# Performance work log

Measured on AMD Instinct MI355X. Metric: run time of the kernel, lower is better.

## Reference

```python
import jax, jax.numpy as jnp
import numpy as np

N, F, H, C, HX, E = 50000, 256, 128, 16, 64, 500000
TEMP = 1.0


def gcn_conv(x, src, dst, W, b, n):
    # PyG GCNConv: x @ W, add self-loops, sym-normalized scatter-sum src->dst
    xw = x @ W
    idx = jnp.arange(n)
    s = jnp.concatenate([src, idx])
    d = jnp.concatenate([dst, idx])
    deg = jax.ops.segment_sum(jnp.ones_like(s, dtype=xw.dtype), d, num_segments=n)
    dinv = jnp.where(deg > 0, jax.lax.rsqrt(deg), 0.0)
    norm = dinv[s] * dinv[d]
    out = jax.ops.segment_sum(xw[s] * norm[:, None], d, num_segments=n)
    return out + b


def setup_inputs() -> dict:
    key = jax.random.key(0)
    ks = jax.random.split(key, 16)
    x = jax.random.normal(ks[0], (N, F), jnp.float32)
    edge_index = jax.random.randint(ks[1], (2, E), 0, N)
    neg_edge_index = jax.random.randint(ks[2], (2, E), 0, N)
    y = jax.random.randint(ks[3], (N,), 0, C)
    train_mask = jax.random.uniform(ks[4], (N,)) < 0.5
    def lin(k, fi, fo):
        s = 1.0 / np.sqrt(fi)
        return jax.random.uniform(k, (fi, fo), jnp.float32, -s, s)
    W1 = lin(ks[5], F, H); b1 = jnp.zeros((H,), jnp.float32)
    W2 = lin(ks[6], H, C); b2 = jnp.zeros((C,), jnp.float32)
    Wx = lin(ks[7], F, HX); bx = jnp.zeros((HX,), jnp.float32)
    Wd = lin(ks[8], 2 * (HX + C), 1); bd = jnp.zeros((1,), jnp.float32)
    return dict(x=x, edge_index=edge_index, neg_edge_index=neg_edge_index, y=y,
                train_mask=train_mask, W1=W1, b1=b1, W2=W2, b2=b2,
                Wx=Wx, bx=bx, Wd=Wd, bd=bd)


def reference(x, edge_index, neg_edge_index, y, train_mask,
              W1, b1, W2, b2, Wx, bx, Wd, bd):
    n = x.shape[0]
    # GNN encoder p(y|x,G): 2-layer GCN (eval mode -> dropout identity)
    h = jax.nn.relu(gcn_conv(x, edge_index[0], edge_index[1], W1, b1, n))
    logits = gcn_conv(h, edge_index[0], edge_index[1], W2, b2, n) / TEMP
    y_log_prob = jax.nn.log_softmax(logits, axis=-1)
    y_prob = jnp.where(train_mask[:, None],
                       jax.nn.one_hot(y, logits.shape[-1], dtype=logits.dtype),
                       jnp.exp(y_log_prob))
    # node feature encoder
    xe = jax.nn.relu(x @ Wx + bx)
    def decode(ei):
        s, d = ei[0], ei[1]
        feat = jnp.concatenate([xe[s], xe[d], y_prob[s], y_prob[d]], axis=1)
        return feat @ Wd + bd
    e_pred_pos = decode(edge_index)
    e_pred_neg = decode(neg_edge_index)
    return e_pred_pos, e_pred_neg, y_log_prob
```

## Files before the change

### kernel.cpp

```cpp
#include <hip/hip_runtime.h>

typedef unsigned short ushort_t;
typedef __attribute__((ext_vector_type(8))) short short8;
typedef __attribute__((ext_vector_type(4))) float floatx4;

constexpr int F = 256, H = 128, C = 16, HX = 64;
constexpr int NBCOL = H + HX;

__device__ __forceinline__ ushort_t f2bf(float f) {
  unsigned u = __float_as_uint(f);
  u += 0x7fffu + ((u >> 16) & 1u);
  return (ushort_t)(u >> 16);
}
__device__ __forceinline__ float bflo(unsigned u) { return __uint_as_float(u << 16); }
__device__ __forceinline__ float bfhi(unsigned u) { return __uint_as_float(u & 0xffff0000u); }

__global__ void k_pre(const float* __restrict__ x, ushort_t* __restrict__ xb, int totalU,
                      const float* __restrict__ W1, const float* __restrict__ Wx,
                      ushort_t* __restrict__ WBt,
                      const int* __restrict__ dst, int* __restrict__ deg, int e,
                      int n, int nbx, int nbw) {
  int b = blockIdx.x;
  if (b < nbx) {
    int i = b * 256 + threadIdx.x;
    if (i >= totalU) return;
    int tile = i >> 9, rem = i & 511, j = rem >> 4, l15 = rem & 15;
    int row = tile * 16 + l15;
    ushort4 lo = make_ushort4(0, 0, 0, 0), hi = lo;
    if (row < n) {
      const float4* xp = (const float4*)(x + (size_t)row * F + j * 8);
      float4 a = xp[0], bb = xp[1];
      lo = make_ushort4(f2bf(a.x), f2bf(a.y), f2bf(a.z), f2bf(a.w));
      hi = make_ushort4(f2bf(bb.x), f2bf(bb.y), f2bf(bb.z), f2bf(bb.w));
    }
    ((ushort4*)xb)[2 * i] = lo;
    ((ushort4*)xb)[2 * i + 1] = hi;
  } else if (b < nbx + nbw) {
    int i = (b - nbx) * 256 + threadIdx.x;
    if (i >= NBCOL * F) return;
    int nn = i / F, k = i % F;
    float v = (nn < H) ? W1[k * H + nn] : Wx[k * HX + (nn - H)];
    WBt[nn * F + k] = f2bf(v);
  } else {
    int i = (b - nbx - nbw) * 256 + threadIdx.x;
    if (i < e) atomicAdd(&deg[dst[i]], 1);
  }
}

__global__ void k_scan_a(const int* __restrict__ deg, int* __restrict__ part, int n) {
  __shared__ int sm[256];
  int i = blockIdx.x * 256 + threadIdx.x;
  int v = (i < n) ? deg[i] : 0;
  sm[threadIdx.x] = v;
  __syncthreads();
  for (int s = 128; s > 0; s >>= 1) {
    if (threadIdx.x < s) sm[threadIdx.x] += sm[threadIdx.x + s];
    __syncthreads();
  }
  if (threadIdx.x == 0) part[blockIdx.x] = sm[0];
}

__global__ void k_scan_c(const int* __restrict__ deg, const int* __restrict__ part,
                         int* __restrict__ row_start, int* __restrict__ cursor,
                         float* __restrict__ dinv, int n, int e) {
  __shared__ int psm[256];
  __shared__ int wsum[4], woff[4];
  int c = blockIdx.x, t = threadIdx.x;
  psm[t] = (t < c) ? part[t] : 0;
  __syncthreads();
  for (int s = 128; s > 0; s >>= 1) {
    if (t < s) psm[t] += psm[t + s];
    __syncthreads();
  }
  int blockoff = psm[0];
  __syncthreads();

  int i = c * 256 + t;
  int lane = t & 63, wid = t >> 6;
  int v = (i < n) ? deg[i] : 0;
  int xs = v;
  for (int d = 1; d < 64; d <<= 1) {
    int u = __shfl_up(xs, d);
    if (lane >= d) xs += u;
  }
  if (lane == 63) wsum[wid] = xs;
  __syncthreads();
  if (t == 0) {
    int s = 0;
    for (int w = 0; w < 4; w++) { woff[w] = s; s += wsum[w]; }
  }
  __syncthreads();
  int excl = xs - v + woff[wid] + blockoff;
  if (i < n) {
    row_start[i] = excl;
    cursor[i] = excl;
    dinv[i] = rsqrtf((float)(v + 1));
  }
  if (i == 0) row_start[n] = e;
}

__global__ void k_fill(const int* __restrict__ src, const int* __restrict__ dst,
                       const float* __restrict__ dinv, int* __restrict__ cursor,
                       int2* __restrict__ csr8, int e) {
  int i = blockIdx.x * 256 + threadIdx.x;
  if (i < e) {
    int s = src[i];
    int p = atomicAdd(&cursor[dst[i]], 1);
    csr8[p] = make_int2(s, __float_as_int(dinv[s]));
  }
}

__global__ __launch_bounds__(256, 3) void k_gemm1(const ushort_t* __restrict__ xb,
                                                  const ushort_t* __restrict__ WBt,
                                                  const float* __restrict__ bx,
                                                  ushort_t* __restrict__ xw1,
                                                  float* __restrict__ xe,
                                                  int n, int ntiles) {
  int w = threadIdx.x >> 6, lane = threadIdx.x & 63;
  int q = lane >> 4, l15 = lane & 15;
  const short8* bb = (const short8*)WBt;
  short8 bfr[3][8];
#pragma unroll
  for (int t = 0; t < 3; t++)
#pragma unroll
    for (int kk = 0; kk < 8; kk++)
      bfr[t][kk] = bb[(size_t)(w * 48 + t * 16 + l15) * 32 + kk * 4 + q];

  float bxv[3];
#pragma unroll
  for (int t = 0; t < 3; t++) {
    int g = w * 48 + t * 16;
    bxv[t] = (g >= H) ? bx[g - H + l15] : 0.0f;
  }

  const short8* ab = (const short8*)xb;
  for (int tile = blockIdx.x; tile < ntiles; tile += gridDim.x) {
    const short8* atile = ab + (size_t)tile * 512;
    short8 a[8];
#pragma unroll
    for (int kk = 0; kk < 8; kk++) a[kk] = atile[kk * 64 + q * 16 + l15];

    floatx4 acc0 = (floatx4)(0.0f), acc1 = (floatx4)(0.0f), acc2 = (floatx4)(0.0f);
#pragma unroll
    for (int kk = 0; kk < 8; kk++) {
      acc0 = __builtin_amdgcn_mfma_f32_16x16x32_bf16(a[kk], bfr[0][kk], acc0, 0, 0, 0);
      acc1 = __builtin_amdgcn_mfma_f32_16x16x32_bf16(a[kk], bfr[1][kk], acc1, 0, 0, 0);
      acc2 = __builtin_amdgcn_mfma_f32_16x16x32_bf16(a[kk], bfr[2][kk], acc2, 0, 0, 0);
    }

    floatx4 accs[3] = {acc0, acc1, acc2};
    int rbase = tile * 16 + q * 4;
#pragma unroll
    for (int t = 0; t < 3; t++) {
      int g = w * 48 + t * 16;
#pragma unroll
      for (int r = 0; r < 4; r++) {
        int ro = rbase + r;
        if (ro < n) {
          if (g < H) {
            xw1[(size_t)ro * H + g + l15] = f2bf(accs[t][r]);
          } else {
            xe[(size_t)ro * HX + (g - H) + l15] = fmaxf(accs[t][r] + bxv[t], 0.0f);
          }
        }
      }
    }
  }
}

__global__ void k_agg1g2(const ushort_t* __restrict__ xw1, const int* __restrict__ row_start,
                         const int2* __restrict__ csr8, const float* __restrict__ dinv,
                         const float* __restrict__ b1, const float* __restrict__ W2,
                         float* __restrict__ hw2, int n) {
  __shared__ float2 hsm[4][64];
  int wid = threadIdx.x >> 6;
  int v = blockIdx.x * 4 + wid;
  if (v >= n) return;
  int lane = threadIdx.x & 63;
  float dv = dinv[v];
  unsigned sv = ((const unsigned*)(xw1 + (size_t)v * H))[lane];
  float ax = dv * bflo(sv), ay = dv * bfhi(sv);
  int j0 = row_start[v], j1 = row_start[v + 1];
  int j = j0;
  for (; j + 8 <= j1; j += 8) {
    int2 ee[8];
    unsigned rr[8];
#pragma unroll
    for (int u = 0; u < 8; u++) ee[u] = csr8[j + u];
#pragma unroll
    for (int u = 0; u < 8; u++)
      rr[u] = ((const unsigned*)(xw1 + (size_t)ee[u].x * H))[lane];
#pragma unroll
    for (int u = 0; u < 8; u++) {
      float wu = __int_as_float(ee[u].y);
      ax += wu * bflo(rr[u]);
      ay += wu * bfhi(rr[u]);
    }
  }
  for (; j < j1; j++) {
    int2 e0 = csr8[j];
    unsigned r0 = ((const unsigned*)(xw1 + (size_t)e0.x * H))[lane];
    float w0 = __int_as_float(e0.y);
    ax += w0 * bflo(r0);
    ay += w0 * bfhi(r0);
  }
  int c2 = lane * 2;
  float o0 = fmaxf(dv * ax + b1[c2], 0.0f);
  float o1 = fmaxf(dv * ay + b1[c2 + 1], 0.0f);
  hsm[wid][lane] = make_float2(o0, o1);

  int c = lane & 15, g = lane >> 4;
  const float* hrow = (const float*)hsm[wid];
  float p = 0.0f;
#pragma unroll
  for (int jj = 0; jj < 32; jj++)
    p += hrow[g * 32 + jj] * W2[(g * 32 + jj) * C + c];
  p += __shfl_xor(p, 16);
  p += __shfl_xor(p, 32);
  if (g == 0) hw2[(size_t)v * C + c] = p;
}

__global__ void k_agg2ab(const float* __restrict__ hw2, const int* __restrict__ row_start,
                         const int2* __restrict__ csr8, const float* __restrict__ dinv,
                         const float* __restrict__ b2, const int* __restrict__ y,
                         const int* __restrict__ tmask, const float* __restrict__ xe,
                         const float* __restrict__ Wd, float* __restrict__ ylp_out,
                         float* __restrict__ Aarr, float* __restrict__ Barr, int n) {
  int idx = blockIdx.x * 256 + threadIdx.x;
  int node = idx >> 4, c = idx & 15;
  if (node >= n) return;
  float dv = dinv[node];
  float acc = dv * hw2[(size_t)node * C + c];
  int j0 = row_start[node], j1 = row_start[node + 1];
  int j = j0;
  for (; j + 8 <= j1; j += 8) {
    int2 ee[8];
    float rr[8];
#pragma unroll
    for (int u = 0; u < 8; u++) ee[u] = csr8[j + u];
#pragma unroll
    for (int u = 0; u < 8; u++) rr[u] = hw2[(size_t)ee[u].x * C + c];
#pragma unroll
    for (int u = 0; u < 8; u++) acc += __int_as_float(ee[u].y) * rr[u];
  }
  for (; j + 4 <= j1; j += 4) {
    int2 e0 = csr8[j], e1 = csr8[j + 1], e2 = csr8[j + 2], e3 = csr8[j + 3];
    float r0 = hw2[(size_t)e0.x * C + c];
    float r1 = hw2[(size_t)e1.x * C + c];
    float r2 = hw2[(size_t)e2.x * C + c];
    float r3 = hw2[(size_t)e3.x * C + c];
    acc += __int_as_float(e0.y) * r0 + __int_as_float(e1.y) * r1 +
           __int_as_float(e2.y) * r2 + __int_as_float(e3.y) * r3;
  }
  for (; j < j1; j++) {
    int2 e0 = csr8[j];
    acc += __int_as_float(e0.y) * hw2[(size_t)e0.x * C + c];
  }
  float logit = dv * acc + b2[c];
  float m = logit;
  for (int o = 8; o > 0; o >>= 1) m = fmaxf(m, __shfl_xor(m, o, 16));
  float e = expf(logit - m);
  float s16 = e;
  for (int o = 8; o > 0; o >>= 1) s16 += __shfl_xor(s16, o, 16);
  float lp = (logit - m) - logf(s16);
  ylp_out[(size_t)node * C + c] = lp;
  float yp = tmask[node] ? ((y[node] == c) ? 1.0f : 0.0f) : (e / s16);

  float4 xv = *(const float4*)(xe + (size_t)node * HX + c * 4);
  float4 wa = *(const float4*)(Wd + c * 4);
  float4 wb = *(const float4*)(Wd + HX + c * 4);
  float pa = xv.x * wa.x + xv.y * wa.y + xv.z * wa.z + xv.w * wa.w + yp * Wd[2 * HX + c];
  float pb = xv.x * wb.x + xv.y * wb.y + xv.z * wb.z + xv.w * wb.w + yp * Wd[2 * HX + C + c];
  for (int o = 8; o > 0; o >>= 1) {
    pa += __shfl_xor(pa, o, 16);
    pb += __shfl_xor(pb, o, 16);
  }
  if (c == 0) { Aarr[node] = pa; Barr[node] = pb; }
}

__global__ void k_decode(const int* __restrict__ ei, const int* __restrict__ nei,
                         const float* __restrict__ Aarr, const float* __restrict__ Barr,
                         const float* __restrict__ bd, float* __restrict__ out, int e) {
  int i = blockIdx.x * 256 + threadIdx.x;
  if (i >= 2 * e) return;
  float b0 = bd[0];
  if (i < e) {
    int s = ei[i], d = ei[e + i];
    out[i] = Aarr[s] + Barr[d] + b0;
  } else {
    int j = i - e;
    int s = nei[j], d = nei[e + j];
    out[e + j] = Aarr[s] + Barr[d] + b0;
  }
}

extern "C" void kernel_launch(void* const* d_in, const int* in_sizes, int n_in,
                              void* d_out, int out_size, void* d_ws, size_t ws_size,
                              hipStream_t stream) {
  const float* x = (const float*)d_in[0];
  const int* ei = (const int*)d_in[1];
  const int* nei = (const int*)d_in[2];
  const int* y = (const int*)d_in[3];
  const int* tmask = (const int*)d_in[4];
  const float* W1 = (const float*)d_in[5];
  const float* b1 = (const float*)d_in[6];
  const float* W2 = (const float*)d_in[7];
  const float* b2 = (const float*)d_in[8];
  const float* Wx = (const float*)d_in[9];
  const float* bx = (const float*)d_in[10];
  const float* Wd = (const float*)d_in[11];
  const float* bd = (const float*)d_in[12];
  float* out = (float*)d_out;

  int n = in_sizes[3];
  int e = in_sizes[1] / 2;
  int ntiles = (n + 15) / 16;

  char* ws = (char*)d_ws;
  size_t off = 0;
  auto alloc = [&](size_t bytes) -> void* {
    void* p = ws + off;
    off += (bytes + 511) & ~(size_t)511;
    return p;
  };
  int* deg = (int*)alloc((size_t)n * 4);
  ushort_t* xb = (ushort_t*)alloc((size_t)ntiles * 16 * F * 2);
  ushort_t* WBt = (ushort_t*)alloc((size_t)NBCOL * F * 2);
  ushort_t* xw1 = (ushort_t*)alloc((size_t)n * H * 2);
  float* xe = (float*)alloc((size_t)n * HX * 4);
  float* hw2 = (float*)alloc((size_t)n * C * 4);
  float* dinv = (float*)alloc((size_t)n * 4);
  int* row_start = (int*)alloc((size_t)(n + 1) * 4);
  int* cursor = (int*)alloc((size_t)n * 4);
  int2* csr8 = (int2*)alloc((size_t)e * 8);
  int* part = (int*)alloc(1024 * 4);
  float* Aarr = (float*)alloc((size_t)n * 4);
  float* Barr = (float*)alloc((size_t)n * 4);

  const int* src = ei;
  const int* dst = ei + e;

  hipMemsetAsync(deg, 0, (size_t)n * 4, stream);

  int totalU = ntiles * 512;
  int nbx = (totalU + 255) / 256;
  int nbw = (NBCOL * F + 255) / 256;
  int nbe = (e + 255) / 256;
  k_pre<<<nbx + nbw + nbe, 256, 0, stream>>>(x, xb, totalU, W1, Wx, WBt, dst, deg, e,
                                             n, nbx, nbw);

  int nchunk = (n + 255) / 256;
  k_scan_a<<<nchunk, 256, 0, stream>>>(deg, part, n);
  k_scan_c<<<nchunk, 256, 0, stream>>>(deg, part, row_start, cursor, dinv, n, e);
  k_fill<<<(e + 255) / 256, 256, 0, stream>>>(src, dst, dinv, cursor, csr8, e);

  int ggrid = ntiles < 768 ? ntiles : 768;
  k_gemm1<<<ggrid, 256, 0, stream>>>(xb, WBt, bx, xw1, xe, n, ntiles);
  k_agg1g2<<<(n + 3) / 4, 256, 0, stream>>>(xw1, row_start, csr8, dinv, b1, W2, hw2, n);
  k_agg2ab<<<(n * 16 + 255) / 256, 256, 0, stream>>>(hw2, row_start, csr8, dinv, b2, y,
                                                     tmask, xe, Wd, out + (size_t)2 * e,
                                                     Aarr, Barr, n);
  k_decode<<<(2 * e + 255) / 256, 256, 0, stream>>>(ei, nei, Aarr, Barr, bd, out, e);
}
```

Before: 252.9 us.

## Merge scan kernels, unroll aggregation tails, vectorize edge decode

Replaces the two-pass degree scan with a single kernel where each block sums all preceding degrees directly. This removes one launch and the partials buffer but adds redundant reads that grow with block index. The aggregation tail loops become unrolled 4/2/1 steps to shorten the serial remainder. The decode kernel now handles two edges per thread with int2 index loads and float2 stores when the edge count is even.

```diff
diff --git a/kernel.cpp b/kernel.cpp
--- a/kernel.cpp
+++ b/kernel.cpp
@@ -47,26 +47,16 @@
   }
 }
 
-__global__ void k_scan_a(const int* __restrict__ deg, int* __restrict__ part, int n) {
-  __shared__ int sm[256];
-  int i = blockIdx.x * 256 + threadIdx.x;
-  int v = (i < n) ? deg[i] : 0;
-  sm[threadIdx.x] = v;
-  __syncthreads();
-  for (int s = 128; s > 0; s >>= 1) {
-    if (threadIdx.x < s) sm[threadIdx.x] += sm[threadIdx.x + s];
-    __syncthreads();
-  }
-  if (threadIdx.x == 0) part[blockIdx.x] = sm[0];
-}
-
-__global__ void k_scan_c(const int* __restrict__ deg, const int* __restrict__ part,
-                         int* __restrict__ row_start, int* __restrict__ cursor,
-                         float* __restrict__ dinv, int n, int e) {
+__global__ void k_scan(const int* __restrict__ deg,
+                       int* __restrict__ row_start, int* __restrict__ cursor,
+                       float* __restrict__ dinv, int n, int e) {
   __shared__ int psm[256];
   __shared__ int wsum[4], woff[4];
   int c = blockIdx.x, t = threadIdx.x;
-  psm[t] = (t < c) ? part[t] : 0;
+  int base = c * 256;
+  int accs = 0;
+  for (int i = t; i < base; i += 256) accs += deg[i];
+  psm[t] = accs;
   __syncthreads();
   for (int s = 128; s > 0; s >>= 1) {
     if (t < s) psm[t] += psm[t + s];
@@ -75,7 +65,7 @@
   int blockoff = psm[0];
   __syncthreads();
 
-  int i = c * 256 + t;
+  int i = base + t;
   int lane = t & 63, wid = t >> 6;
   int v = (i < n) ? deg[i] : 0;
   int xs = v;
@@ -197,7 +187,32 @@
       ay += wu * bfhi(rr[u]);
     }
   }
-  for (; j < j1; j++) {
+  if (j + 4 <= j1) {
+    int2 ee[4];
+    unsigned rr[4];
+#pragma unroll
+    for (int u = 0; u < 4; u++) ee[u] = csr8[j + u];
+#pragma unroll
+    for (int u = 0; u < 4; u++)
+      rr[u] = ((const unsigned*)(xw1 + (size_t)ee[u].x * H))[lane];
+#pragma unroll
+    for (int u = 0; u < 4; u++) {
+      float wu = __int_as_float(ee[u].y);
+      ax += wu * bflo(rr[u]);
+      ay += wu * bfhi(rr[u]);
+    }
+    j += 4;
+  }
+  if (j + 2 <= j1) {
+    int2 e0 = csr8[j], e1 = csr8[j + 1];
+    unsigned r0 = ((const unsigned*)(xw1 + (size_t)e0.x * H))[lane];
+    unsigned r1 = ((const unsigned*)(xw1 + (size_t)e1.x * H))[lane];
+    float w0 = __int_as_float(e0.y), w1 = __int_as_float(e1.y);
+    ax += w0 * bflo(r0) + w1 * bflo(r1);
+    ay += w0 * bfhi(r0) + w1 * bfhi(r1);
+    j += 2;
+  }
+  if (j < j1) {
     int2 e0 = csr8[j];
     unsigned r0 = ((const unsigned*)(xw1 + (size_t)e0.x * H))[lane];
     float w0 = __int_as_float(e0.y);
@@ -243,7 +258,7 @@
 #pragma unroll
     for (int u = 0; u < 8; u++) acc += __int_as_float(ee[u].y) * rr[u];
   }
-  for (; j + 4 <= j1; j += 4) {
+  if (j + 4 <= j1) {
     int2 e0 = csr8[j], e1 = csr8[j + 1], e2 = csr8[j + 2], e3 = csr8[j + 3];
     float r0 = hw2[(size_t)e0.x * C + c];
     float r1 = hw2[(size_t)e1.x * C + c];
@@ -251,8 +266,16 @@
     float r3 = hw2[(size_t)e3.x * C + c];
     acc += __int_as_float(e0.y) * r0 + __int_as_float(e1.y) * r1 +
            __int_as_float(e2.y) * r2 + __int_as_float(e3.y) * r3;
-  }
-  for (; j < j1; j++) {
+    j += 4;
+  }
+  if (j + 2 <= j1) {
+    int2 e0 = csr8[j], e1 = csr8[j + 1];
+    float r0 = hw2[(size_t)e0.x * C + c];
+    float r1 = hw2[(size_t)e1.x * C + c];
+    acc += __int_as_float(e0.y) * r0 + __int_as_float(e1.y) * r1;
+    j += 2;
+  }
+  if (j < j1) {
     int2 e0 = csr8[j];
     acc += __int_as_float(e0.y) * hw2[(size_t)e0.x * C + c];
   }
@@ -281,16 +304,33 @@
 __global__ void k_decode(const int* __restrict__ ei, const int* __restrict__ nei,
                          const float* __restrict__ Aarr, const float* __restrict__ Barr,
                          const float* __restrict__ bd, float* __restrict__ out, int e) {
-  int i = blockIdx.x * 256 + threadIdx.x;
-  if (i >= 2 * e) return;
   float b0 = bd[0];
-  if (i < e) {
-    int s = ei[i], d = ei[e + i];
-    out[i] = Aarr[s] + Barr[d] + b0;
+  if ((e & 1) == 0) {
+    int half = e >> 1;
+    int i = blockIdx.x * 256 + threadIdx.x;
+    if (i >= 2 * half) return;
+    if (i < half) {
+      int j = 2 * i;
+      int2 s2 = *(const int2*)(ei + j);
+      int2 d2 = *(const int2*)(ei + e + j);
+      *(float2*)(out + j) =
+          make_float2(Aarr[s2.x] + Barr[d2.x] + b0, Aarr[s2.y] + Barr[d2.y] + b0);
+    } else {
+      int j = 2 * (i - half);
+      int2 s2 = *(const int2*)(nei + j);
+      int2 d2 = *(const int2*)(nei + e + j);
+      *(float2*)(out + e + j) =
+          make_float2(Aarr[s2.x] + Barr[d2.x] + b0, Aarr[s2.y] + Barr[d2.y] + b0);
+    }
   } else {
-    int j = i - e;
-    int s = nei[j], d = nei[e + j];
-    out[e + j] = Aarr[s] + Barr[d] + b0;
+    int i = blockIdx.x * 256 + threadIdx.x;
+    if (i >= 2 * e) return;
+    if (i < e) {
+      out[i] = Aarr[ei[i]] + Barr[ei[e + i]] + b0;
+    } else {
+      int j = i - e;
+      out[e + j] = Aarr[nei[j]] + Barr[nei[e + j]] + b0;
+    }
   }
 }
 
@@ -333,7 +373,6 @@
   int* row_start = (int*)alloc((size_t)(n + 1) * 4);
   int* cursor = (int*)alloc((size_t)n * 4);
   int2* csr8 = (int2*)alloc((size_t)e * 8);
-  int* part = (int*)alloc(1024 * 4);
   float* Aarr = (float*)alloc((size_t)n * 4);
   float* Barr = (float*)alloc((size_t)n * 4);
 
@@ -350,8 +389,7 @@
                                              n, nbx, nbw);
 
   int nchunk = (n + 255) / 256;
-  k_scan_a<<<nchunk, 256, 0, stream>>>(deg, part, n);
-  k_scan_c<<<nchunk, 256, 0, stream>>>(deg, part, row_start, cursor, dinv, n, e);
+  k_scan<<<nchunk, 256, 0, stream>>>(deg, row_start, cursor, dinv, n, e);
   k_fill<<<(e + 255) / 256, 256, 0, stream>>>(src, dst, dinv, cursor, csr8, e);
 
   int ggrid = ntiles < 768 ? ntiles : 768;
@@ -360,5 +398,6 @@
   k_agg2ab<<<(n * 16 + 255) / 256, 256, 0, stream>>>(hw2, row_start, csr8, dinv, b2, y,
                                                      tmask, xe, Wd, out + (size_t)2 * e,
                                                      Aarr, Barr, n);
-  k_decode<<<(2 * e + 255) / 256, 256, 0, stream>>>(ei, nei, Aarr, Barr, bd, out, e);
-}
+  int dthreads = ((e & 1) == 0) ? e : 2 * e;
+  k_decode<<<(dthreads + 255) / 256, 256, 0, stream>>>(ei, nei, Aarr, Barr, bd, out, e);
+}
```

Measured after the change: 269.0 us. 1.06x slower.
